# Optimization experiments

Hardware: AMD Instinct MI355X
Metric: run time of the kernel (lower is better)

## Reference

```python
import jax, jax.numpy as jnp
import numpy as np

HIDDEN = 512
NHEADS = 8
ALPHA = 0.1
NUM_HOP = 4
MASK_VAL = -16384.0
LN_EPS = 1e-5


def setup_inputs() -> dict:
    key = jax.random.key(0)
    ks = jax.random.split(key, 10)
    B, N, H = 8, 1024, HIDDEN
    s = 1.0 / np.sqrt(H)
    x = jax.random.normal(ks[0], (B, N, H), dtype=jnp.float32)
    adj = jax.random.randint(ks[1], (B, N, N), 0, 2, dtype=jnp.int32)
    Wq = jax.random.uniform(ks[2], (H, H), jnp.float32, -s, s)
    bq = jax.random.uniform(ks[3], (H,), jnp.float32, -s, s)
    Wk = jax.random.uniform(ks[4], (H, H), jnp.float32, -s, s)
    bk = jax.random.uniform(ks[5], (H,), jnp.float32, -s, s)
    Wv = jax.random.uniform(ks[6], (H, H), jnp.float32, -s, s)
    bv = jax.random.uniform(ks[7], (H,), jnp.float32, -s, s)
    gamma = jnp.ones((H,), jnp.float32)
    beta = jnp.zeros((H,), jnp.float32)
    return {"x": x, "adj": adj, "Wq": Wq, "bq": bq, "Wk": Wk, "bk": bk,
            "Wv": Wv, "bv": bv, "gamma": gamma, "beta": beta}


def reference(x, adj, Wq, bq, Wk, bk, Wv, bv, gamma, beta):
    B, N, H = x.shape
    u = H // NHEADS
    # torch Linear: y = x @ W^T + b
    q = x @ Wq.T + bq  # [B,N,H]
    k = x @ Wk.T + bk
    v = x @ Wv.T + bv
    # split hidden into contiguous head chunks (matches per-head slicing)
    qh = q.reshape(B, N, NHEADS, u).transpose(0, 2, 1, 3)  # [B,Hd,N,u]
    kh = k.reshape(B, N, NHEADS, u).transpose(0, 2, 1, 3)
    vh = v.reshape(B, N, NHEADS, u).transpose(0, 2, 1, 3)
    scores = jnp.einsum('bhnd,bhmd->bhnm', qh, kh)  # [B,Hd,N,N]
    mask = (adj == 0)[:, None, :, :]  # broadcast over heads
    scores = jnp.where(mask, MASK_VAL, scores)
    pros = jax.nn.softmax(scores, axis=-1)
    z_init = vh
    z = z_init
    for _ in range(NUM_HOP):
        z = (1.0 - ALPHA) * jnp.einsum('bhnm,bhmd->bhnd', pros, z) + ALPHA * z_init
    h_prime = z.transpose(0, 2, 1, 3).reshape(B, N, H)  # concat heads
    y = x + h_prime
    mu = jnp.mean(y, axis=-1, keepdims=True)
    var = jnp.mean((y - mu) ** 2, axis=-1, keepdims=True)
    return (y - mu) / jnp.sqrt(var + LN_EPS) * gamma + beta
```

## Files before the change

kernel.cpp:

```cpp
#include <hip/hip_runtime.h>
#include <hip/hip_bf16.h>

#define BB 8
#define NN 1024
#define HH 512
#define NHEADS 8
#define UU 64

typedef __attribute__((ext_vector_type(8))) short short8;
typedef __attribute__((ext_vector_type(4))) float f32x4;
typedef unsigned short u16;
typedef unsigned char u8;

__device__ inline float b2f(unsigned short u) {
    union { float f; unsigned int i; } c; c.i = ((unsigned int)u) << 16; return c.f;
}
__device__ inline unsigned short f2b(float f) {
    __hip_bfloat16 h = __float2bfloat16(f);
    return *reinterpret_cast<unsigned short*>(&h);
}
__device__ inline void gl_lds16(const void* g, void* l) {
    __builtin_amdgcn_global_load_lds(
        (const __attribute__((address_space(1))) unsigned int*)g,
        (__attribute__((address_space(3))) unsigned int*)l, 16, 0, 0);
}
__device__ inline u8 f2fp8(float f) {
    return (u8)__builtin_amdgcn_cvt_pk_fp8_f32(f, f, 0, false);
}

__global__ __launch_bounds__(256) void cvt_bf16(
    const float* __restrict__ x, const float* __restrict__ Wq,
    const float* __restrict__ Wk, const float* __restrict__ Wv,
    u16* __restrict__ xb, u16* __restrict__ Wb)
{
    const int which = blockIdx.y;
    const float* src;
    u16* dst;
    int n;
    if (which == 0) { src = x;  dst = xb;              n = BB * NN * HH; }
    else if (which == 1) { src = Wq; dst = Wb;             n = HH * HH; }
    else if (which == 2) { src = Wk; dst = Wb + HH * HH;   n = HH * HH; }
    else              { src = Wv; dst = Wb + 2 * HH * HH;  n = HH * HH; }

    const int base = (blockIdx.x * 256 + threadIdx.x) * 8;
    if (base >= n) return;
    const float4* sp = (const float4*)&src[base];
    float4 a = sp[0], b = sp[1];
    short8 o;
    o[0] = (short)f2b(a.x); o[1] = (short)f2b(a.y);
    o[2] = (short)f2b(a.z); o[3] = (short)f2b(a.w);
    o[4] = (short)f2b(b.x); o[5] = (short)f2b(b.y);
    o[6] = (short)f2b(b.z); o[7] = (short)f2b(b.w);
    *(short8*)&dst[base] = o;
}

__global__ __launch_bounds__(256) void adj_pack(
    const int* __restrict__ adj, unsigned int* __restrict__ adjp)
{
    const int wave = threadIdx.x >> 6, lane = threadIdx.x & 63;
    const int row = blockIdx.x * 4 + wave;
    const int* ar = adj + (size_t)row * NN;
    unsigned long long* out = (unsigned long long*)(adjp + (size_t)row * 32);
    #pragma unroll
    for (int it = 0; it < 16; ++it) {
        int a = ar[it * 64 + lane];
        unsigned long long m = __ballot(a != 0);
        if (lane == 0) out[it] = m;
    }
}

__global__ __launch_bounds__(256) void qkv_gemm(
    const u16* __restrict__ xb, const u16* __restrict__ Wb,
    const float* __restrict__ bq, const float* __restrict__ bk,
    const float* __restrict__ bv,
    u16* __restrict__ q, u16* __restrict__ k, u16* __restrict__ v)
{
    const int which = blockIdx.z;
    const u16* W      = Wb + which * HH * HH;
    const float* bias = which == 0 ? bq : (which == 1 ? bk : bv);
    u16* out          = which == 0 ? q  : (which == 1 ? k  : v);

    const int tid = threadIdx.x;
    const int wave = tid >> 6, lane = tid & 63;
    const int ln = lane & 15, quad = lane >> 4;
    const int wr = (wave >> 1) * 64, wc = (wave & 1) * 64;
    const int rowbase = blockIdx.x * 128, colbase = blockIdx.y * 128;

    __shared__ __align__(16) u16 As[128 * 32];
    __shared__ __align__(16) u16 Bs[128 * 32];

    f32x4 acc[4][4];
    #pragma unroll
    for (int ri = 0; ri < 4; ++ri)
        #pragma unroll
        for (int ci = 0; ci < 4; ++ci) acc[ri][ci] = (f32x4){0.f, 0.f, 0.f, 0.f};

    const int lr = lane >> 2;
    const int lk = (lane & 3) * 8;

    for (int kk = 0; kk < HH; kk += 32) {
        __syncthreads();
        #pragma unroll
        for (int i = 0; i < 2; ++i) {
            int r = wave * 32 + i * 16 + lr;
            gl_lds16(&xb[(size_t)(rowbase + r) * HH + kk + lk],
                     (char*)As + (wave * 32 + i * 16) * 64);
            gl_lds16(&W[(size_t)(colbase + r) * HH + kk + lk],
                     (char*)Bs + (wave * 32 + i * 16) * 64);
        }
        __syncthreads();

        short8 bfr[4];
        #pragma unroll
        for (int ci = 0; ci < 4; ++ci)
            bfr[ci] = *(const short8*)&Bs[(wc + ci * 16 + ln) * 32 + quad * 8];
        #pragma unroll
        for (int ri = 0; ri < 4; ++ri) {
            short8 af = *(const short8*)&As[(wr + ri * 16 + ln) * 32 + quad * 8];
            #pragma unroll
            for (int ci = 0; ci < 4; ++ci)
                acc[ri][ci] = __builtin_amdgcn_mfma_f32_16x16x32_bf16(af, bfr[ci], acc[ri][ci], 0, 0, 0);
        }
    }

    #pragma unroll
    for (int ci = 0; ci < 4; ++ci) {
        int col = colbase + wc + ci * 16 + ln;
        int hh = col >> 6, dd = col & 63;
        float bb = bias[col];
        #pragma unroll
        for (int ri = 0; ri < 4; ++ri) {
            #pragma unroll
            for (int r = 0; r < 4; ++r) {
                int row = rowbase + wr + ri * 16 + quad * 4 + r;
                int bidx = row >> 10, n = row & 1023;
                out[(((size_t)(bidx * NHEADS + hh)) * NN + n) * UU + dd] = f2b(acc[ri][ci][r] + bb);
            }
        }
    }
}

__global__ __launch_bounds__(256) void scores_softmax(
    const u16* __restrict__ q, const u16* __restrict__ kmat,
    const unsigned int* __restrict__ adjp, u8* __restrict__ P8)
{
    const int b = blockIdx.z, h = blockIdx.y, rt = blockIdx.x;
    const int bh = b * NHEADS + h;
    const int wave = threadIdx.x >> 6, lane = threadIdx.x & 63;
    const int ln = lane & 15, quad = lane >> 4;
    const int rowbase = rt * 16;

    __shared__ float redsum[4][16];
    __shared__ __align__(16) u8 Pst[16384];

    const u16* qp = &q[((size_t)bh * NN + rowbase + ln) * UU + quad * 8];
    short8 a0 = *(const short8*)qp;
    short8 a1 = *(const short8*)(qp + 32);

    unsigned int abits[4][8];
    #pragma unroll
    for (int r = 0; r < 4; ++r) {
        int row = rowbase + quad * 4 + r;
        const uint4* ap = (const uint4*)&adjp[((size_t)(b * NN + row)) * 32 + wave * 8];
        *(uint4*)&abits[r][0] = ap[0];
        *(uint4*)&abits[r][4] = ap[1];
    }

    f32x4 accs[16];
    #pragma unroll
    for (int ct = 0; ct < 16; ++ct) {
        int col = wave * 256 + ct * 16 + ln;
        const u16* kp = &kmat[((size_t)bh * NN + col) * UU + quad * 8];
        short8 b0 = *(const short8*)kp;
        short8 b1 = *(const short8*)(kp + 32);
        f32x4 acc = (f32x4){0.f, 0.f, 0.f, 0.f};
        acc = __builtin_amdgcn_mfma_f32_16x16x32_bf16(a0, b0, acc, 0, 0, 0);
        acc = __builtin_amdgcn_mfma_f32_16x16x32_bf16(a1, b1, acc, 0, 0, 0);
        accs[ct] = acc;
    }

    float rsum[4] = {0.f, 0.f, 0.f, 0.f};
    #pragma unroll
    for (int ct = 0; ct < 16; ++ct) {
        const int kc8 = ct >> 1;
        const int bitpos = (ct & 1) * 16 + ln;
        #pragma unroll
        for (int r = 0; r < 4; ++r) {
            unsigned int on = (abits[r][kc8] >> bitpos) & 1u;
            float e = on ? __expf(accs[ct][r] - 32.0f) : 0.0f;
            accs[ct][r] = e;
            rsum[r] += e;
        }
    }
    #pragma unroll
    for (int r = 0; r < 4; ++r) {
        #pragma unroll
        for (int off = 8; off >= 1; off >>= 1)
            rsum[r] += __shfl_xor(rsum[r], off);
    }
    if (ln == 0) {
        #pragma unroll
        for (int r = 0; r < 4; ++r) redsum[wave][quad * 4 + r] = rsum[r];
    }
    __syncthreads();
    float sc16[4];
    #pragma unroll
    for (int r = 0; r < 4; ++r) {
        int row16 = quad * 4 + r;
        float s = redsum[0][row16] + redsum[1][row16] + redsum[2][row16] + redsum[3][row16];
        sc16[r] = 16.0f / s;
    }

    #pragma unroll
    for (int ct = 0; ct < 16; ++ct) {
        int kc = wave * 8 + (ct >> 1);
        int cb = (ct & 1) * 16 + ln;
        #pragma unroll
        for (int r = 0; r < 4; ++r)
            Pst[kc * 512 + (quad * 4 + r) * 32 + cb] = f2fp8(accs[ct][r] * sc16[r]);
    }
    __syncthreads();

    u8* Pb = P8 + ((size_t)bh << 20) + rt * 16384;
    const uint4* srcp = (const uint4*)(Pst + threadIdx.x * 64);
    uint4* dstp = (uint4*)(Pb + threadIdx.x * 64);
    dstp[0] = srcp[0]; dstp[1] = srcp[1]; dstp[2] = srcp[2]; dstp[3] = srcp[3];
}

__global__ __launch_bounds__(256) void vt8(
    const u16* __restrict__ v, u8* __restrict__ v8t)
{
    const int bh = blockIdx.x;
    const int t = threadIdx.x;
    const size_t hd = (size_t)bh << 16;
    __shared__ u16 tile[64][72];

    for (int chunk = 0; chunk < 16; ++chunk) {
        const int n0 = chunk * 64;
        const int r = t >> 2, cs = t & 3;
        const u16* vp = &v[((size_t)bh * NN + n0 + r) * UU + cs * 16];
        short8 a = *(const short8*)vp;
        short8 b8 = *(const short8*)(vp + 8);
        #pragma unroll
        for (int j = 0; j < 8; ++j) {
            tile[r][cs * 16 + j] = (u16)a[j];
            tile[r][cs * 16 + 8 + j] = (u16)b8[j];
        }
        __syncthreads();
        const int c = t & 63, qt = t >> 6;
        unsigned int w[4];
        #pragma unroll
        for (int g = 0; g < 4; ++g) {
            float f0 = b2f(tile[qt * 16 + g * 4 + 0][c]);
            float f1 = b2f(tile[qt * 16 + g * 4 + 1][c]);
            float f2 = b2f(tile[qt * 16 + g * 4 + 2][c]);
            float f3 = b2f(tile[qt * 16 + g * 4 + 3][c]);
            int lo = __builtin_amdgcn_cvt_pk_fp8_f32(f0, f1, 0, false);
            w[g] = (unsigned int)__builtin_amdgcn_cvt_pk_fp8_f32(f2, f3, lo, true);
        }
        uint4 o; o.x = w[0]; o.y = w[1]; o.z = w[2]; o.w = w[3];
        *(uint4*)&v8t[hd + (size_t)c * 1024 + n0 + qt * 16] = o;
        __syncthreads();
    }
}

__global__ __launch_bounds__(512) void hop(
    const u8* __restrict__ P8, const u8* __restrict__ z8in,
    const u16* __restrict__ v, u8* __restrict__ z8out,
    u16* __restrict__ zbf_out, int last)
{
    const int b = blockIdx.z, h = blockIdx.y, rt = blockIdx.x;
    const int bh = b * NHEADS + h;
    const int tid = threadIdx.x;
    const int wave = tid >> 6, lane = tid & 63;
    const int ln = lane & 15, quad = lane >> 4;
    const int wrow = rt * 128 + wave * 16;

    __shared__ __align__(16) u8 zt[64 * 1040];

    const u8* zg = z8in + ((size_t)bh << 16);
    #pragma unroll
    for (int i = 0; i < 8; ++i) {
        int c = wave * 8 + i;
        gl_lds16(zg + (size_t)c * 1024 + lane * 16, (char*)zt + c * 1040);
    }
    __syncthreads();

    f32x4 acc[4];
    #pragma unroll
    for (int ci = 0; ci < 4; ++ci) acc[ci] = (f32x4){0.f, 0.f, 0.f, 0.f};

    const u8* pt = P8 + ((size_t)bh << 20) + (size_t)(rt * 8 + wave) * 16384
                 + ln * 32 + quad * 8;
    #pragma unroll 4
    for (int kc = 0; kc < 32; ++kc) {
        long a = *(const long*)(pt + kc * 512);
        int kk = kc * 32;
        #pragma unroll
        for (int ci = 0; ci < 4; ++ci) {
            long bz = *(const long*)&zt[(ci * 16 + ln) * 1040 + kk + quad * 8];
            acc[ci] = __builtin_amdgcn_mfma_f32_16x16x32_fp8_fp8(a, bz, acc[ci], 0, 0, 0);
        }
    }

    if (last) {
        #pragma unroll
        for (int ci = 0; ci < 4; ++ci) {
            int col = ci * 16 + ln;
            #pragma unroll
            for (int r = 0; r < 4; ++r) {
                int row = wrow + quad * 4 + r;
                float vv = b2f(v[((size_t)bh * NN + row) * UU + col]);
                zbf_out[((size_t)(b * NN + row)) * HH + h * UU + col]
                    = f2b(0.05625f * acc[ci][r] + 0.1f * vv);
            }
        }
    } else {
        u8* zo = z8out + ((size_t)bh << 16);
        #pragma unroll
        for (int ci = 0; ci < 4; ++ci) {
            int col = ci * 16 + ln;
            float zv[4];
            #pragma unroll
            for (int r = 0; r < 4; ++r) {
                int row = wrow + quad * 4 + r;
                float vv = b2f(v[((size_t)bh * NN + row) * UU + col]);
                zv[r] = 0.05625f * acc[ci][r] + 0.1f * vv;
            }
            int lo = __builtin_amdgcn_cvt_pk_fp8_f32(zv[0], zv[1], 0, false);
            unsigned int dw = (unsigned int)__builtin_amdgcn_cvt_pk_fp8_f32(zv[2], zv[3], lo, true);
            *(unsigned int*)&zo[(size_t)col * 1024 + wrow + quad * 4] = dw;
        }
    }
}

__global__ __launch_bounds__(256) void resid_ln(
    const float* __restrict__ x, const u16* __restrict__ z,
    const float* __restrict__ gamma, const float* __restrict__ beta,
    float* __restrict__ out)
{
    const int r = blockIdx.x * 4 + (threadIdx.x >> 6);
    const int lane = threadIdx.x & 63;
    const size_t base = (size_t)r * HH + lane * 8;

    const float4* xp = (const float4*)&x[base];
    float4 x0 = xp[0], x1 = xp[1];
    short8 zv = *(const short8*)&z[base];
    float y[8];
    y[0] = x0.x + b2f((u16)zv[0]); y[1] = x0.y + b2f((u16)zv[1]);
    y[2] = x0.z + b2f((u16)zv[2]); y[3] = x0.w + b2f((u16)zv[3]);
    y[4] = x1.x + b2f((u16)zv[4]); y[5] = x1.y + b2f((u16)zv[5]);
    y[6] = x1.z + b2f((u16)zv[6]); y[7] = x1.w + b2f((u16)zv[7]);

    float s = 0.f, sq = 0.f;
    #pragma unroll
    for (int j = 0; j < 8; ++j) { s += y[j]; sq += y[j] * y[j]; }
    #pragma unroll
    for (int off = 32; off >= 1; off >>= 1) {
        s  += __shfl_xor(s, off);
        sq += __shfl_xor(sq, off);
    }
    const float mu = s * (1.0f / HH);
    const float var = sq * (1.0f / HH) - mu * mu;
    const float rstd = rsqrtf(var + 1e-5f);

    const float4* gp = (const float4*)&gamma[lane * 8];
    const float4* bp = (const float4*)&beta[lane * 8];
    float4 g0 = gp[0], g1 = gp[1], b0 = bp[0], b1 = bp[1];

    float4 o0, o1;
    o0.x = (y[0] - mu) * rstd * g0.x + b0.x;
    o0.y = (y[1] - mu) * rstd * g0.y + b0.y;
    o0.z = (y[2] - mu) * rstd * g0.z + b0.z;
    o0.w = (y[3] - mu) * rstd * g0.w + b0.w;
    o1.x = (y[4] - mu) * rstd * g1.x + b1.x;
    o1.y = (y[5] - mu) * rstd * g1.y + b1.y;
    o1.z = (y[6] - mu) * rstd * g1.z + b1.z;
    o1.w = (y[7] - mu) * rstd * g1.w + b1.w;
    float4* op = (float4*)&out[base];
    op[0] = o0; op[1] = o1;
}

extern "C" void kernel_launch(void* const* d_in, const int* in_sizes, int n_in,
                              void* d_out, int out_size, void* d_ws, size_t ws_size,
                              hipStream_t stream)
{
    const float* x   = (const float*)d_in[0];
    const int* adj   = (const int*)d_in[1];
    const float* Wq  = (const float*)d_in[2];
    const float* bq  = (const float*)d_in[3];
    const float* Wk  = (const float*)d_in[4];
    const float* bk  = (const float*)d_in[5];
    const float* Wv  = (const float*)d_in[6];
    const float* bv  = (const float*)d_in[7];
    const float* gamma = (const float*)d_in[8];
    const float* beta  = (const float*)d_in[9];
    float* out = (float*)d_out;

    const size_t E = (size_t)BB * NN * HH;
    u16* ws16 = (u16*)d_ws;
    u16* xb = ws16;
    u16* q  = ws16 + E;
    u16* k  = ws16 + 2 * E;
    u16* v  = ws16 + 3 * E;
    u16* za = ws16 + 4 * E;
    u16* Wb = ws16 + 5 * E;
    u8* base8 = (u8*)(ws16 + 5 * E + 786432);
    u8* P8  = base8;
    u8* z8a = base8 + ((size_t)64 << 20);
    u8* z8b = z8a + ((size_t)4 << 20);
    u8* v8t = z8b + ((size_t)4 << 20);
    unsigned int* adjp = (unsigned int*)(v8t + ((size_t)4 << 20));

    cvt_bf16<<<dim3(2048, 4), 256, 0, stream>>>(x, Wq, Wk, Wv, xb, Wb);
    adj_pack<<<dim3(2048), 256, 0, stream>>>(adj, adjp);
    qkv_gemm<<<dim3(64, 4, 3), 256, 0, stream>>>(xb, Wb, bq, bk, bv, q, k, v);
    scores_softmax<<<dim3(64, NHEADS, BB), 256, 0, stream>>>(q, k, adjp, P8);
    vt8<<<dim3(64), 256, 0, stream>>>(v, v8t);
    hop<<<dim3(8, NHEADS, BB), 512, 0, stream>>>(P8, v8t, v, z8a, za, 0);
    hop<<<dim3(8, NHEADS, BB), 512, 0, stream>>>(P8, z8a, v, z8b, za, 0);
    hop<<<dim3(8, NHEADS, BB), 512, 0, stream>>>(P8, z8b, v, z8a, za, 0);
    hop<<<dim3(8, NHEADS, BB), 512, 0, stream>>>(P8, z8a, v, z8b, za, 1);
    resid_ln<<<dim3(2048), 256, 0, stream>>>(x, za, gamma, beta, out);
}
```

Baseline: 304.9 us.

## Fuse first propagation hop into scores softmax and stage QKV stores through LDS

The first hop (P @ V) is now computed inside the scores/softmax kernel using the FP8 probability tile already held in shared memory, so one hop launch and one re-read of P from global memory go away. vt8 now runs before the scores kernel to provide the transposed FP8 V. Separately, the QKV GEMM epilogue writes its tile to an LDS buffer and then issues coalesced 16-byte row stores instead of scattered 2-byte stores. The trade-offs are more LDS per QKV block, which may lower occupancy, and extra MFMA work plus V loads in the scores kernel. The hard-coded 0.05625 factor has to match the scale used for the FP8 P values.

```diff
diff --git a/kernel.cpp b/kernel.cpp
--- a/kernel.cpp
+++ b/kernel.cpp
@@ -88,6 +88,7 @@
 
     __shared__ __align__(16) u16 As[128 * 32];
     __shared__ __align__(16) u16 Bs[128 * 32];
+    __shared__ __align__(16) u16 Cs[128 * 136];
 
     f32x4 acc[4][4];
     #pragma unroll
@@ -125,24 +126,74 @@
 
     #pragma unroll
     for (int ci = 0; ci < 4; ++ci) {
-        int col = colbase + wc + ci * 16 + ln;
-        int hh = col >> 6, dd = col & 63;
-        float bb = bias[col];
+        int col = wc + ci * 16 + ln;
+        float bb = bias[colbase + col];
         #pragma unroll
         for (int ri = 0; ri < 4; ++ri) {
             #pragma unroll
             for (int r = 0; r < 4; ++r) {
-                int row = rowbase + wr + ri * 16 + quad * 4 + r;
-                int bidx = row >> 10, n = row & 1023;
-                out[(((size_t)(bidx * NHEADS + hh)) * NN + n) * UU + dd] = f2b(acc[ri][ci][r] + bb);
+                int row = wr + ri * 16 + quad * 4 + r;
+                Cs[row * 136 + col] = f2b(acc[ri][ci][r] + bb);
             }
         }
     }
-}
-
-__global__ __launch_bounds__(256) void scores_softmax(
+    __syncthreads();
+
+    {
+        int row = tid >> 1, half = tid & 1;
+        int gcol0 = colbase + half * 64;
+        int hh = gcol0 >> 6;
+        int grow = rowbase + row;
+        int bidx = grow >> 10, n = grow & 1023;
+        u16* op = &out[(((size_t)(bidx * NHEADS + hh)) * NN + n) * UU];
+        const u16* cp = &Cs[row * 136 + half * 64];
+        #pragma unroll
+        for (int j = 0; j < 8; ++j)
+            *(short8*)(op + j * 8) = *(const short8*)(cp + j * 8);
+    }
+}
+
+__global__ __launch_bounds__(256) void vt8(
+    const u16* __restrict__ v, u8* __restrict__ v8t)
+{
+    const int bh = blockIdx.x;
+    const int t = threadIdx.x;
+    const size_t hd = (size_t)bh << 16;
+    __shared__ u16 tile[64][72];
+
+    for (int chunk = 0; chunk < 16; ++chunk) {
+        const int n0 = chunk * 64;
+        const int r = t >> 2, cs = t & 3;
+        const u16* vp = &v[((size_t)bh * NN + n0 + r) * UU + cs * 16];
+        short8 a = *(const short8*)vp;
+        short8 b8 = *(const short8*)(vp + 8);
+        #pragma unroll
+        for (int j = 0; j < 8; ++j) {
+            tile[r][cs * 16 + j] = (u16)a[j];
+            tile[r][cs * 16 + 8 + j] = (u16)b8[j];
+        }
+        __syncthreads();
+        const int c = t & 63, qt = t >> 6;
+        unsigned int w[4];
+        #pragma unroll
+        for (int g = 0; g < 4; ++g) {
+            float f0 = b2f(tile[qt * 16 + g * 4 + 0][c]);
+            float f1 = b2f(tile[qt * 16 + g * 4 + 1][c]);
+            float f2 = b2f(tile[qt * 16 + g * 4 + 2][c]);
+            float f3 = b2f(tile[qt * 16 + g * 4 + 3][c]);
+            int lo = __builtin_amdgcn_cvt_pk_fp8_f32(f0, f1, 0, false);
+            w[g] = (unsigned int)__builtin_amdgcn_cvt_pk_fp8_f32(f2, f3, lo, true);
+        }
+        uint4 o; o.x = w[0]; o.y = w[1]; o.z = w[2]; o.w = w[3];
+        *(uint4*)&v8t[hd + (size_t)c * 1024 + n0 + qt * 16] = o;
+        __syncthreads();
+    }
+}
+
+__global__ __launch_bounds__(256) void scores_softmax_h1(
     const u16* __restrict__ q, const u16* __restrict__ kmat,
-    const unsigned int* __restrict__ adjp, u8* __restrict__ P8)
+    const unsigned int* __restrict__ adjp, const u8* __restrict__ v8t,
+    const u16* __restrict__ v, u8* __restrict__ P8, u8* __restrict__ z8out)
 {
     const int b = blockIdx.z, h = blockIdx.y, rt = blockIdx.x;
     const int bh = b * NHEADS + h;
@@ -221,46 +272,33 @@
     }
     __syncthreads();
 
-    u8* Pb = P8 + ((size_t)bh << 20) + rt * 16384;
-    const uint4* srcp = (const uint4*)(Pst + threadIdx.x * 64);
-    uint4* dstp = (uint4*)(Pb + threadIdx.x * 64);
-    dstp[0] = srcp[0]; dstp[1] = srcp[1]; dstp[2] = srcp[2]; dstp[3] = srcp[3];
-}
-
-__global__ __launch_bounds__(256) void vt8(
-    const u16* __restrict__ v, u8* __restrict__ v8t)
-{
-    const int bh = blockIdx.x;
-    const int t = threadIdx.x;
-    const size_t hd = (size_t)bh << 16;
-    __shared__ u16 tile[64][72];
-
-    for (int chunk = 0; chunk < 16; ++chunk) {
-        const int n0 = chunk * 64;
-        const int r = t >> 2, cs = t & 3;
-        const u16* vp = &v[((size_t)bh * NN + n0 + r) * UU + cs * 16];
-        short8 a = *(const short8*)vp;
-        short8 b8 = *(const short8*)(vp + 8);
-        #pragma unroll
-        for (int j = 0; j < 8; ++j) {
-            tile[r][cs * 16 + j] = (u16)a[j];
-            tile[r][cs * 16 + 8 + j] = (u16)b8[j];
-        }
-        __syncthreads();
-        const int c = t & 63, qt = t >> 6;
-        unsigned int w[4];
-        #pragma unroll
-        for (int g = 0; g < 4; ++g) {
-            float f0 = b2f(tile[qt * 16 + g * 4 + 0][c]);
-            float f1 = b2f(tile[qt * 16 + g * 4 + 1][c]);
-            float f2 = b2f(tile[qt * 16 + g * 4 + 2][c]);
-            float f3 = b2f(tile[qt * 16 + g * 4 + 3][c]);
-            int lo = __builtin_amdgcn_cvt_pk_fp8_f32(f0, f1, 0, false);
-            w[g] = (unsigned int)__builtin_amdgcn_cvt_pk_fp8_f32(f2, f3, lo, true);
-        }
-        uint4 o; o.x = w[0]; o.y = w[1]; o.z = w[2]; o.w = w[3];
-        *(uint4*)&v8t[hd + (size_t)c * 1024 + n0 + qt * 16] = o;
-        __syncthreads();
+    {
+        u8* Pb = P8 + ((size_t)bh << 20) + rt * 16384;
+        const uint4* srcp = (const uint4*)(Pst + threadIdx.x * 64);
+        uint4* dstp = (uint4*)(Pb + threadIdx.x * 64);
+        dstp[0] = srcp[0]; dstp[1] = srcp[1]; dstp[2] = srcp[2]; dstp[3] = srcp[3];
+    }
+
+    {
+        const u8* vt = v8t + ((size_t)bh << 16);
+        const int dcol = wave * 16 + ln;
+        f32x4 h1 = (f32x4){0.f, 0.f, 0.f, 0.f};
+        #pragma unroll 4
+        for (int kc = 0; kc < 32; ++kc) {
+            long a = *(const long*)&Pst[kc * 512 + ln * 32 + quad * 8];
+            long bz = *(const long*)&vt[(size_t)dcol * 1024 + kc * 32 + quad * 8];
+            h1 = __builtin_amdgcn_mfma_f32_16x16x32_fp8_fp8(a, bz, h1, 0, 0, 0);
+        }
+        const int n0 = rowbase + quad * 4;
+        float zv[4];
+        #pragma unroll
+        for (int r = 0; r < 4; ++r) {
+            float vv = b2f(v[((size_t)bh * NN + n0 + r) * UU + dcol]);
+            zv[r] = 0.05625f * h1[r] + 0.1f * vv;
+        }
+        int lo = __builtin_amdgcn_cvt_pk_fp8_f32(zv[0], zv[1], 0, false);
+        unsigned int dw = (unsigned int)__builtin_amdgcn_cvt_pk_fp8_f32(zv[2], zv[3], lo, true);
+        *(unsigned int*)&z8out[((size_t)bh << 16) + (size_t)dcol * 1024 + n0] = dw;
     }
 }
 
@@ -415,9 +453,8 @@
     cvt_bf16<<<dim3(2048, 4), 256, 0, stream>>>(x, Wq, Wk, Wv, xb, Wb);
     adj_pack<<<dim3(2048), 256, 0, stream>>>(adj, adjp);
     qkv_gemm<<<dim3(64, 4, 3), 256, 0, stream>>>(xb, Wb, bq, bk, bv, q, k, v);
-    scores_softmax<<<dim3(64, NHEADS, BB), 256, 0, stream>>>(q, k, adjp, P8);
     vt8<<<dim3(64), 256, 0, stream>>>(v, v8t);
-    hop<<<dim3(8, NHEADS, BB), 512, 0, stream>>>(P8, v8t, v, z8a, za, 0);
+    scores_softmax_h1<<<dim3(64, NHEADS, BB), 256, 0, stream>>>(q, k, adjp, v8t, v, P8, z8a);
     hop<<<dim3(8, NHEADS, BB), 512, 0, stream>>>(P8, z8a, v, z8b, za, 0);
     hop<<<dim3(8, NHEADS, BB), 512, 0, stream>>>(P8, z8b, v, z8a, za, 0);
     hop<<<dim3(8, NHEADS, BB), 512, 0, stream>>>(P8, z8a, v, z8b, za, 1);
```

Result: slower. 342.8 us (+12.4%).
